# Optimization experiments

Hardware: AMD Instinct MI355X
Metric: run time of the kernel (lower is better)

The kernel has to match this reference:

```python
import jax, jax.numpy as jnp
import numpy as np

N = 100000
E = 1600000
F_IN = 128
H = 128
C = 2


def setup_inputs() -> dict:
    key = jax.random.key(0)
    ks = jax.random.split(key, 12)
    s = lambda fan_in: 1.0 / np.sqrt(fan_in)
    inp = {
        "x": jax.random.normal(ks[0], (N, F_IN), dtype=jnp.float32),
        "edge_index": jax.random.randint(ks[1], (2, E), 0, N, dtype=jnp.int32),
        "edge_weight": jax.random.uniform(ks[2], (E,), dtype=jnp.float32),
        # first_lin: features_num -> hidden
        "W_first": jax.random.uniform(ks[3], (F_IN, H), minval=-s(F_IN), maxval=s(F_IN)),
        "b_first": jnp.zeros((H,), jnp.float32),
        # GRUCell (torch layout: [3*H, H] for ih and hh)
        "W_ih": jax.random.uniform(ks[4], (3 * H, H), minval=-s(H), maxval=s(H)),
        "b_ih": jax.random.uniform(ks[5], (3 * H,), minval=-s(H), maxval=s(H)),
        "W_hh": jax.random.uniform(ks[6], (3 * H, H), minval=-s(H), maxval=s(H)),
        "b_hh": jax.random.uniform(ks[7], (3 * H,), minval=-s(H), maxval=s(H)),
        # lin1: hidden -> hidden
        "W_lin1": jax.random.uniform(ks[8], (H, H), minval=-s(H), maxval=s(H)),
        "b_lin1": jnp.zeros((H,), jnp.float32),
        # out: hidden -> num_class
        "W_out": jax.random.uniform(ks[9], (H, C), minval=-s(H), maxval=s(H)),
        "b_out": jnp.zeros((C,), jnp.float32),
    }
    return inp


def _gated_conv(x, edge_index, edge_weight):
    # gather source node features, scale by edge weight, scatter-add to dst
    src, dst = edge_index[0], edge_index[1]
    msg = x[src] * edge_weight[:, None]           # [E, H]
    return jax.ops.segment_sum(msg, dst, num_segments=N)  # [N, H]


def _gru_cell(inp, hid, W_ih, b_ih, W_hh, b_hh):
    gi = inp @ W_ih.T + b_ih                      # [N, 3H]
    gh = hid @ W_hh.T + b_hh                      # [N, 3H]
    i_r, i_z, i_n = jnp.split(gi, 3, axis=-1)
    h_r, h_z, h_n = jnp.split(gh, 3, axis=-1)
    r = jax.nn.sigmoid(i_r + h_r)
    z = jax.nn.sigmoid(i_z + h_z)
    n = jnp.tanh(i_n + r * h_n)
    return (1.0 - z) * n + z * hid


def reference(x, edge_index, edge_weight, W_first, b_first, W_ih, b_ih,
              W_hh, b_hh, W_lin1, b_lin1, W_out, b_out):
    x = x @ W_first + b_first                     # [N, H] (dropout: eval mode no-op)
    h = x
    x = _gated_conv(x, edge_index, edge_weight)
    x = _gru_cell(x, h, W_ih, b_ih, W_hh, b_hh)
    x = x @ W_lin1 + b_lin1
    x = _gated_conv(x, edge_index, edge_weight)
    x = _gru_cell(x, h, W_ih, b_ih, W_hh, b_hh)
    logits = x @ W_out + b_out                    # [N, C]
    return jax.nn.log_softmax(logits, axis=-1)
```

## Files before the change

### kernel.cpp

```cpp
#include <hip/hip_runtime.h>
#include <hip/hip_bf16.h>

#define H 128
#define SCAN_T 256
#define SCAN_I 8
#define SCAN_CHUNK (SCAN_T * SCAN_I)

typedef __bf16 bf16_t;
typedef __attribute__((ext_vector_type(2))) __bf16 bf16x2;
typedef __attribute__((ext_vector_type(8))) __bf16 bf16x8;
typedef __attribute__((ext_vector_type(4))) float f32x4;

static_assert(sizeof(bf16x8) == 16, "bf16x8 must be 16 bytes");

__device__ inline bf16x8 load_a_frag_f32(const float* __restrict__ A, int row, int koff) {
    const float4* p = (const float4*)(A + (size_t)row * H + koff);
    float4 v0 = p[0], v1 = p[1];
    bf16x8 r;
    r[0] = (bf16_t)v0.x; r[1] = (bf16_t)v0.y; r[2] = (bf16_t)v0.z; r[3] = (bf16_t)v0.w;
    r[4] = (bf16_t)v1.x; r[5] = (bf16_t)v1.y; r[6] = (bf16_t)v1.z; r[7] = (bf16_t)v1.w;
    return r;
}

__global__ void prep_weights(const float* __restrict__ Wf,  const float* __restrict__ Wih,
                             const float* __restrict__ Whh, const float* __restrict__ Wl1,
                             bf16_t* __restrict__ wfT, bf16_t* __restrict__ wih,
                             bf16_t* __restrict__ whh, bf16_t* __restrict__ wl1T) {
    int i = blockIdx.x * blockDim.x + threadIdx.x;
    if (i < 128 * 128) {
        int c = i >> 7, k = i & 127;
        wfT[i]  = (bf16_t)Wf[k * 128 + c];
        wl1T[i] = (bf16_t)Wl1[k * 128 + c];
    }
    if (i < 384 * 128) {
        wih[i] = (bf16_t)Wih[i];
        whh[i] = (bf16_t)Whh[i];
    }
}

__global__ void hist_kernel(const int* __restrict__ ei, int* __restrict__ deg, int nE) {
    int e = blockIdx.x * blockDim.x + threadIdx.x;
    if (e < nE) atomicAdd(&deg[ei[nE + e]], 1);
}

__global__ __launch_bounds__(SCAN_T) void scan1_kernel(
    const int* __restrict__ deg, int* __restrict__ rowptr, int* __restrict__ bsum, int n) {
    __shared__ int s[SCAN_T];
    int base = blockIdx.x * SCAN_CHUNK + threadIdx.x * SCAN_I;
    int v[SCAN_I];
    int sum = 0;
    for (int j = 0; j < SCAN_I; ++j) {
        int idx = base + j;
        v[j] = (idx < n) ? deg[idx] : 0;
        sum += v[j];
    }
    s[threadIdx.x] = sum;
    __syncthreads();
    for (int off = 1; off < SCAN_T; off <<= 1) {
        int t = (threadIdx.x >= off) ? s[threadIdx.x - off] : 0;
        __syncthreads();
        s[threadIdx.x] += t;
        __syncthreads();
    }
    int run = s[threadIdx.x] - sum;
    for (int j = 0; j < SCAN_I; ++j) {
        int idx = base + j;
        if (idx < n) rowptr[idx] = run;
        run += v[j];
    }
    if (threadIdx.x == SCAN_T - 1) bsum[blockIdx.x] = s[SCAN_T - 1];
}

__global__ __launch_bounds__(SCAN_T) void scan2_kernel(int* __restrict__ bsum, int nb) {
    __shared__ int s[SCAN_T];
    int v = (threadIdx.x < nb) ? bsum[threadIdx.x] : 0;
    s[threadIdx.x] = v;
    __syncthreads();
    for (int off = 1; off < SCAN_T; off <<= 1) {
        int t = (threadIdx.x >= off) ? s[threadIdx.x - off] : 0;
        __syncthreads();
        s[threadIdx.x] += t;
        __syncthreads();
    }
    if (threadIdx.x < nb) bsum[threadIdx.x] = s[threadIdx.x] - v;
}

__global__ void scan3_kernel(int* __restrict__ rowptr, int* __restrict__ cursor,
                             const int* __restrict__ bsum, int n, int nE) {
    int idx = blockIdx.x * blockDim.x + threadIdx.x;
    if (idx < n) {
        int val = rowptr[idx] + bsum[idx / SCAN_CHUNK];
        rowptr[idx] = val;
        cursor[idx] = val;
    }
    if (idx == 0) rowptr[n] = nE;
}

__global__ void scatter_kernel(const int* __restrict__ ei, const float* __restrict__ ew,
                               int* __restrict__ cursor, int2* __restrict__ srcw, int nE) {
    int e = blockIdx.x * blockDim.x + threadIdx.x;
    if (e < nE) {
        int src = ei[e], dst = ei[nE + e];
        float w = ew[e];
        int pos = atomicAdd(&cursor[dst], 1);
        srcw[pos] = make_int2(src, __float_as_int(w));
    }
}

__device__ inline void conv_fma(float* acc, uint4 u, float w) {
    acc[0] += __uint_as_float(u.x << 16) * w;
    acc[1] += __uint_as_float(u.x & 0xffff0000u) * w;
    acc[2] += __uint_as_float(u.y << 16) * w;
    acc[3] += __uint_as_float(u.y & 0xffff0000u) * w;
    acc[4] += __uint_as_float(u.z << 16) * w;
    acc[5] += __uint_as_float(u.z & 0xffff0000u) * w;
    acc[6] += __uint_as_float(u.w << 16) * w;
    acc[7] += __uint_as_float(u.w & 0xffff0000u) * w;
}

__global__ __launch_bounds__(256) void conv_csr_kernel(
    const bf16_t* __restrict__ xb, const int* __restrict__ rowptr,
    const int2* __restrict__ srcw, bf16_t* __restrict__ agg, int n) {
    int lane = threadIdx.x & 63;
    int d = (blockIdx.x * blockDim.x + threadIdx.x) >> 6;
    if (d >= n) return;
    int q = lane >> 4;
    int l = lane & 15;
    int beg = rowptr[d], end = rowptr[d + 1];

    float acc[8];
    #pragma unroll
    for (int i = 0; i < 8; ++i) acc[i] = 0.f;

    int e = beg + q;
    for (; e + 4 < end; e += 8) {
        int2 sw0 = srcw[e];
        int2 sw1 = srcw[e + 4];
        uint4 u0 = *(const uint4*)(xb + (size_t)sw0.x * H + l * 8);
        uint4 u1 = *(const uint4*)(xb + (size_t)sw1.x * H + l * 8);
        conv_fma(acc, u0, __int_as_float(sw0.y));
        conv_fma(acc, u1, __int_as_float(sw1.y));
    }
    if (e < end) {
        int2 sw = srcw[e];
        uint4 u = *(const uint4*)(xb + (size_t)sw.x * H + l * 8);
        conv_fma(acc, u, __int_as_float(sw.y));
    }

    #pragma unroll
    for (int i = 0; i < 8; ++i) {
        acc[i] += __shfl_xor(acc[i], 16);
        acc[i] += __shfl_xor(acc[i], 32);
    }
    if (q == 0) {
        bf16x8 r;
        #pragma unroll
        for (int i = 0; i < 8; ++i) r[i] = (bf16_t)acc[i];
        *(bf16x8*)(agg + (size_t)d * H + l * 8) = r;
    }
}

__global__ __launch_bounds__(256) void lin_first_kernel(
    const float* __restrict__ A, const bf16_t* __restrict__ Bt,
    const float* __restrict__ bias, float* __restrict__ outf,
    bf16_t* __restrict__ outb, int n) {
    int wid = threadIdx.x >> 6, lane = threadIdx.x & 63;
    int r0 = (blockIdx.x * 4 + wid) * 32;
    if (r0 >= n) return;
    int lrow = lane & 15, lk8 = (lane >> 4) * 8;

    bf16x8 a[2][4];
    for (int rt = 0; rt < 2; ++rt) {
        int row = r0 + rt * 16 + lrow;
        if (row >= n) row = n - 1;
        for (int t = 0; t < 4; ++t) a[rt][t] = load_a_frag_f32(A, row, t * 32 + lk8);
    }
    for (int ct = 0; ct < 8; ++ct) {
        int c0 = ct * 16;
        f32x4 acc0 = {0.f, 0.f, 0.f, 0.f}, acc1 = {0.f, 0.f, 0.f, 0.f};
        const bf16_t* bp = Bt + (size_t)(c0 + lrow) * H + lk8;
        for (int t = 0; t < 4; ++t) {
            bf16x8 b = *(const bf16x8*)(bp + t * 32);
            acc0 = __builtin_amdgcn_mfma_f32_16x16x32_bf16(a[0][t], b, acc0, 0, 0, 0);
            acc1 = __builtin_amdgcn_mfma_f32_16x16x32_bf16(a[1][t], b, acc1, 0, 0, 0);
        }
        int col = c0 + lrow;
        float bv = bias[col];
        for (int r = 0; r < 4; ++r) {
            int row0 = r0 + (lane >> 4) * 4 + r;
            float v0 = acc0[r] + bv;
            if (row0 < n) { outf[(size_t)row0 * H + col] = v0; outb[(size_t)row0 * H + col] = (bf16_t)v0; }
            int row1 = row0 + 16;
            float v1 = acc1[r] + bv;
            if (row1 < n) { outf[(size_t)row1 * H + col] = v1; outb[(size_t)row1 * H + col] = (bf16_t)v1; }
        }
    }
}

__global__ __launch_bounds__(256) void lin_mid_kernel(
    const bf16_t* __restrict__ A, const bf16_t* __restrict__ Bt,
    const float* __restrict__ bias, bf16_t* __restrict__ out, int n) {
    int wid = threadIdx.x >> 6, lane = threadIdx.x & 63;
    int r0 = (blockIdx.x * 4 + wid) * 32;
    if (r0 >= n) return;
    int lrow = lane & 15, lk8 = (lane >> 4) * 8;

    bf16x8 a[2][4];
    for (int rt = 0; rt < 2; ++rt) {
        int row = r0 + rt * 16 + lrow;
        if (row >= n) row = n - 1;
        for (int t = 0; t < 4; ++t)
            a[rt][t] = *(const bf16x8*)(A + (size_t)row * H + t * 32 + lk8);
    }
    for (int ct = 0; ct < 8; ++ct) {
        int c0 = ct * 16;
        f32x4 acc0 = {0.f, 0.f, 0.f, 0.f}, acc1 = {0.f, 0.f, 0.f, 0.f};
        const bf16_t* bp = Bt + (size_t)(c0 + lrow) * H + lk8;
        for (int t = 0; t < 4; ++t) {
            bf16x8 b = *(const bf16x8*)(bp + t * 32);
            acc0 = __builtin_amdgcn_mfma_f32_16x16x32_bf16(a[0][t], b, acc0, 0, 0, 0);
            acc1 = __builtin_amdgcn_mfma_f32_16x16x32_bf16(a[1][t], b, acc1, 0, 0, 0);
        }
        int col = c0 + lrow;
        float bv = bias[col];
        for (int r = 0; r < 4; ++r) {
            int row0 = r0 + (lane >> 4) * 4 + r;
            if (row0 < n) out[(size_t)row0 * H + col] = (bf16_t)(acc0[r] + bv);
            int row1 = row0 + 16;
            if (row1 < n) out[(size_t)row1 * H + col] = (bf16_t)(acc1[r] + bv);
        }
    }
}

template<bool LOGITS>
__global__ __launch_bounds__(256) void gru_kernel(
    const bf16_t* __restrict__ inp, const bf16_t* __restrict__ hidb,
    const float* __restrict__ hidf,
    const bf16_t* __restrict__ Wih, const bf16_t* __restrict__ Whh,
    const float* __restrict__ bih, const float* __restrict__ bhh,
    bf16_t* __restrict__ out, const float* __restrict__ Wo,
    const float* __restrict__ bo, float* __restrict__ logits, int n) {
    int wid = threadIdx.x >> 6, lane = threadIdx.x & 63;
    int r0 = (blockIdx.x * 4 + wid) * 32;
    if (r0 >= n) return;
    int lrow = lane & 15, lk8 = (lane >> 4) * 8;

    bf16x8 ai[2][4], ah[2][4];
    for (int rt = 0; rt < 2; ++rt) {
        int row = r0 + rt * 16 + lrow;
        if (row >= n) row = n - 1;
        for (int t = 0; t < 4; ++t) {
            ai[rt][t] = *(const bf16x8*)(inp  + (size_t)row * H + t * 32 + lk8);
            ah[rt][t] = *(const bf16x8*)(hidb + (size_t)row * H + t * 32 + lk8);
        }
    }

    float s0[2][4], s1[2][4];
    if (LOGITS) {
        for (int rt = 0; rt < 2; ++rt)
            for (int r = 0; r < 4; ++r) { s0[rt][r] = 0.f; s1[rt][r] = 0.f; }
    }

    for (int ct = 0; ct < 8; ++ct) {
        int c0 = ct * 16;
        int col = c0 + lrow;
        f32x4 air[2], aiz[2], ain[2], ahr[2], ahz[2], ahn[2];
        for (int rt = 0; rt < 2; ++rt) {
            air[rt] = (f32x4){0.f,0.f,0.f,0.f}; aiz[rt] = (f32x4){0.f,0.f,0.f,0.f};
            ain[rt] = (f32x4){0.f,0.f,0.f,0.f}; ahr[rt] = (f32x4){0.f,0.f,0.f,0.f};
            ahz[rt] = (f32x4){0.f,0.f,0.f,0.f}; ahn[rt] = (f32x4){0.f,0.f,0.f,0.f};
        }
        const bf16_t* pir = Wih + (size_t)(col)       * H + lk8;
        const bf16_t* piz = Wih + (size_t)(128 + col) * H + lk8;
        const bf16_t* pin = Wih + (size_t)(256 + col) * H + lk8;
        const bf16_t* phr = Whh + (size_t)(col)       * H + lk8;
        const bf16_t* phz = Whh + (size_t)(128 + col) * H + lk8;
        const bf16_t* phn = Whh + (size_t)(256 + col) * H + lk8;
        for (int t = 0; t < 4; ++t) {
            bf16x8 bir = *(const bf16x8*)(pir + t * 32);
            bf16x8 biz = *(const bf16x8*)(piz + t * 32);
            bf16x8 bin = *(const bf16x8*)(pin + t * 32);
            bf16x8 bhr = *(const bf16x8*)(phr + t * 32);
            bf16x8 bhz = *(const bf16x8*)(phz + t * 32);
            bf16x8 bhn = *(const bf16x8*)(phn + t * 32);
            for (int rt = 0; rt < 2; ++rt) {
                air[rt] = __builtin_amdgcn_mfma_f32_16x16x32_bf16(ai[rt][t], bir, air[rt], 0, 0, 0);
                aiz[rt] = __builtin_amdgcn_mfma_f32_16x16x32_bf16(ai[rt][t], biz, aiz[rt], 0, 0, 0);
                ain[rt] = __builtin_amdgcn_mfma_f32_16x16x32_bf16(ai[rt][t], bin, ain[rt], 0, 0, 0);
                ahr[rt] = __builtin_amdgcn_mfma_f32_16x16x32_bf16(ah[rt][t], bhr, ahr[rt], 0, 0, 0);
                ahz[rt] = __builtin_amdgcn_mfma_f32_16x16x32_bf16(ah[rt][t], bhz, ahz[rt], 0, 0, 0);
                ahn[rt] = __builtin_amdgcn_mfma_f32_16x16x32_bf16(ah[rt][t], bhn, ahn[rt], 0, 0, 0);
            }
        }
        float b_ir = bih[col], b_iz = bih[128 + col], b_in = bih[256 + col];
        float b_hr = bhh[col], b_hz = bhh[128 + col], b_hn = bhh[256 + col];
        float w0 = 0.f, w1 = 0.f;
        if (LOGITS) { float2 wv = *(const float2*)(Wo + col * 2); w0 = wv.x; w1 = wv.y; }
        for (int rt = 0; rt < 2; ++rt) {
            for (int r = 0; r < 4; ++r) {
                int row = r0 + rt * 16 + (lane >> 4) * 4 + r;
                float irv = air[rt][r] + b_ir, hrv = ahr[rt][r] + b_hr;
                float izv = aiz[rt][r] + b_iz, hzv = ahz[rt][r] + b_hz;
                float inv = ain[rt][r] + b_in, hnv = ahn[rt][r] + b_hn;
                float rg = 1.f / (1.f + __expf(-(irv + hrv)));
                float zg = 1.f / (1.f + __expf(-(izv + hzv)));
                float xx = inv + rg * hnv;
                float ng = 2.f / (1.f + __expf(-2.f * xx)) - 1.f;
                bool ok = (row < n);
                float hv = ok ? hidf[(size_t)row * H + col] : 0.f;
                float hout = (1.f - zg) * ng + zg * hv;
                if (LOGITS) {
                    s0[rt][r] += hout * w0;
                    s1[rt][r] += hout * w1;
                } else if (ok) {
                    out[(size_t)row * H + col] = (bf16_t)hout;
                }
            }
        }
    }

    if (LOGITS) {
        for (int m = 1; m < 16; m <<= 1) {
            for (int rt = 0; rt < 2; ++rt)
                for (int r = 0; r < 4; ++r) {
                    s0[rt][r] += __shfl_xor(s0[rt][r], m);
                    s1[rt][r] += __shfl_xor(s1[rt][r], m);
                }
        }
        if ((lane & 15) == 0) {
            float bo0 = bo[0], bo1 = bo[1];
            for (int rt = 0; rt < 2; ++rt)
                for (int r = 0; r < 4; ++r) {
                    int row = r0 + rt * 16 + (lane >> 4) * 4 + r;
                    if (row < n) {
                        float l0 = s0[rt][r] + bo0, l1 = s1[rt][r] + bo1;
                        float mx = fmaxf(l0, l1);
                        float lse = mx + __logf(__expf(l0 - mx) + __expf(l1 - mx));
                        logits[(size_t)row * 2]     = l0 - lse;
                        logits[(size_t)row * 2 + 1] = l1 - lse;
                    }
                }
        }
    }
}

extern "C" void kernel_launch(void* const* d_in, const int* in_sizes, int n_in,
                              void* d_out, int out_size, void* d_ws, size_t ws_size,
                              hipStream_t stream) {
    const float* x   = (const float*)d_in[0];
    const int*   ei  = (const int*)d_in[1];
    const float* ew  = (const float*)d_in[2];
    const float* Wf  = (const float*)d_in[3];
    const float* bf  = (const float*)d_in[4];
    const float* Wih = (const float*)d_in[5];
    const float* bih = (const float*)d_in[6];
    const float* Whh = (const float*)d_in[7];
    const float* bhh = (const float*)d_in[8];
    const float* Wl1 = (const float*)d_in[9];
    const float* bl1 = (const float*)d_in[10];
    const float* Wo  = (const float*)d_in[11];
    const float* bo  = (const float*)d_in[12];

    int n  = in_sizes[0] / H;
    int nE = in_sizes[2];

    float* hbuf   = (float*)d_ws;
    bf16_t* hbufb = (bf16_t*)(hbuf + (size_t)n * H);
    bf16_t* b1b   = hbufb + (size_t)n * H;
    bf16_t* b2b   = b1b + (size_t)n * H;
    bf16_t* wfT   = b2b + (size_t)n * H;
    bf16_t* wih   = wfT + 128 * 128;
    bf16_t* whh   = wih + 384 * 128;
    bf16_t* wl1T  = whh + 384 * 128;
    int* deg    = (int*)(wl1T + 128 * 128);
    int* rowptr = deg + n;
    int* cursor = rowptr + (n + 1);
    int2* srcw  = (int2*)((char*)(cursor + n) + ((size_t)(-(intptr_t)(cursor + n)) & 7));

    int gemmGrid = (n + 127) / 128;
    int nScanBlocks = (n + SCAN_CHUNK - 1) / SCAN_CHUNK;

    prep_weights<<<192, 256, 0, stream>>>(Wf, Wih, Whh, Wl1, wfT, wih, whh, wl1T);
    hipMemsetAsync(deg, 0, (size_t)n * sizeof(int), stream);
    hist_kernel<<<(nE + 255) / 256, 256, 0, stream>>>(ei, deg, nE);
    scan1_kernel<<<nScanBlocks, SCAN_T, 0, stream>>>(deg, rowptr, cursor, n);
    scan2_kernel<<<1, SCAN_T, 0, stream>>>(cursor, nScanBlocks);
    scan3_kernel<<<(n + 255) / 256, 256, 0, stream>>>(rowptr, deg, cursor, n, nE);
    scatter_kernel<<<(nE + 255) / 256, 256, 0, stream>>>(ei, ew, deg, srcw, nE);

    lin_first_kernel<<<gemmGrid, 256, 0, stream>>>(x, wfT, bf, hbuf, hbufb, n);
    conv_csr_kernel<<<(n + 3) / 4, 256, 0, stream>>>(hbufb, rowptr, srcw, b1b, n);
    gru_kernel<false><<<gemmGrid, 256, 0, stream>>>(b1b, hbufb, hbuf, wih, whh, bih, bhh,
                                                    b1b, nullptr, nullptr, nullptr, n);
    lin_mid_kernel<<<gemmGrid, 256, 0, stream>>>(b1b, wl1T, bl1, b2b, n);
    conv_csr_kernel<<<(n + 3) / 4, 256, 0, stream>>>(b2b, rowptr, srcw, b1b, n);
    gru_kernel<true><<<gemmGrid, 256, 0, stream>>>(b1b, hbufb, hbuf, wih, whh, bih, bhh,
                                                   nullptr, Wo, bo, (float*)d_out, n);
}
```

Baseline: 610.6 us.

## Stage weight matrices in swizzled LDS for linear and GRU MFMA kernels

The linear kernels now copy the whole 128x128 bf16 weight matrix into XOR-swizzled shared memory once per block and read MFMA B fragments from LDS instead of global memory. The GRU kernel double-buffers per-column-tile slices of the six gate weight blocks in LDS, prefetching the next slice into registers while the current one is computed. This targets repeated global/L2 weight fetches by every wave. In exchange it adds 32-48KB of LDS per block, which may lower occupancy, plus block-wide barriers. The early return for out-of-range waves is removed so every thread reaches the barriers.

New measurement: 539.1 us. 11.7% less time.

```diff
diff --git a/kernel.cpp b/kernel.cpp
--- a/kernel.cpp
+++ b/kernel.cpp
@@ -160,14 +160,24 @@
     }
 }
 
+
 __global__ __launch_bounds__(256) void lin_first_kernel(
     const float* __restrict__ A, const bf16_t* __restrict__ Bt,
     const float* __restrict__ bias, float* __restrict__ outf,
     bf16_t* __restrict__ outb, int n) {
-    int wid = threadIdx.x >> 6, lane = threadIdx.x & 63;
+    __shared__ __align__(16) unsigned char wlds[32768];
+    int tid = threadIdx.x;
+    int wid = tid >> 6, lane = tid & 63;
     int r0 = (blockIdx.x * 4 + wid) * 32;
-    if (r0 >= n) return;
-    int lrow = lane & 15, lk8 = (lane >> 4) * 8;
+    int lrow = lane & 15, lq = lane >> 4, lk8 = lq * 8;
+
+    #pragma unroll
+    for (int i = 0; i < 8; ++i) {
+        int g = i * 256 + tid;
+        int row = g >> 4, seg = g & 15;
+        uint4 v = *(const uint4*)(Bt + row * 128 + seg * 8);
+        *(uint4*)(&wlds[row * 256 + ((seg * 16) ^ ((row & 7) << 4))]) = v;
+    }
 
     bf16x8 a[2][4];
     for (int rt = 0; rt < 2; ++rt) {
@@ -175,19 +185,23 @@
         if (row >= n) row = n - 1;
         for (int t = 0; t < 4; ++t) a[rt][t] = load_a_frag_f32(A, row, t * 32 + lk8);
     }
+    __syncthreads();
+
     for (int ct = 0; ct < 8; ++ct) {
         int c0 = ct * 16;
         f32x4 acc0 = {0.f, 0.f, 0.f, 0.f}, acc1 = {0.f, 0.f, 0.f, 0.f};
-        const bf16_t* bp = Bt + (size_t)(c0 + lrow) * H + lk8;
+        int rbase = (c0 + lrow) * 256;
+        int sw = (lrow & 7) << 4;
+        #pragma unroll
         for (int t = 0; t < 4; ++t) {
-            bf16x8 b = *(const bf16x8*)(bp + t * 32);
+            bf16x8 b = *(const bf16x8*)(&wlds[rbase + ((t * 64 + lq * 16) ^ sw)]);
             acc0 = __builtin_amdgcn_mfma_f32_16x16x32_bf16(a[0][t], b, acc0, 0, 0, 0);
             acc1 = __builtin_amdgcn_mfma_f32_16x16x32_bf16(a[1][t], b, acc1, 0, 0, 0);
         }
         int col = c0 + lrow;
         float bv = bias[col];
         for (int r = 0; r < 4; ++r) {
-            int row0 = r0 + (lane >> 4) * 4 + r;
+            int row0 = r0 + lq * 4 + r;
             float v0 = acc0[r] + bv;
             if (row0 < n) { outf[(size_t)row0 * H + col] = v0; outb[(size_t)row0 * H + col] = (bf16_t)v0; }
             int row1 = row0 + 16;
@@ -200,10 +214,19 @@
 __global__ __launch_bounds__(256) void lin_mid_kernel(
     const bf16_t* __restrict__ A, const bf16_t* __restrict__ Bt,
     const float* __restrict__ bias, bf16_t* __restrict__ out, int n) {
-    int wid = threadIdx.x >> 6, lane = threadIdx.x & 63;
+    __shared__ __align__(16) unsigned char wlds[32768];
+    int tid = threadIdx.x;
+    int wid = tid >> 6, lane = tid & 63;
     int r0 = (blockIdx.x * 4 + wid) * 32;
-    if (r0 >= n) return;
-    int lrow = lane & 15, lk8 = (lane >> 4) * 8;
+    int lrow = lane & 15, lq = lane >> 4, lk8 = lq * 8;
+
+    #pragma unroll
+    for (int i = 0; i < 8; ++i) {
+        int g = i * 256 + tid;
+        int row = g >> 4, seg = g & 15;
+        uint4 v = *(const uint4*)(Bt + row * 128 + seg * 8);
+        *(uint4*)(&wlds[row * 256 + ((seg * 16) ^ ((row & 7) << 4))]) = v;
+    }
 
     bf16x8 a[2][4];
     for (int rt = 0; rt < 2; ++rt) {
@@ -212,19 +235,23 @@
         for (int t = 0; t < 4; ++t)
             a[rt][t] = *(const bf16x8*)(A + (size_t)row * H + t * 32 + lk8);
     }
+    __syncthreads();
+
     for (int ct = 0; ct < 8; ++ct) {
         int c0 = ct * 16;
         f32x4 acc0 = {0.f, 0.f, 0.f, 0.f}, acc1 = {0.f, 0.f, 0.f, 0.f};
-        const bf16_t* bp = Bt + (size_t)(c0 + lrow) * H + lk8;
+        int rbase = (c0 + lrow) * 256;
+        int sw = (lrow & 7) << 4;
+        #pragma unroll
         for (int t = 0; t < 4; ++t) {
-            bf16x8 b = *(const bf16x8*)(bp + t * 32);
+            bf16x8 b = *(const bf16x8*)(&wlds[rbase + ((t * 64 + lq * 16) ^ sw)]);
             acc0 = __builtin_amdgcn_mfma_f32_16x16x32_bf16(a[0][t], b, acc0, 0, 0, 0);
             acc1 = __builtin_amdgcn_mfma_f32_16x16x32_bf16(a[1][t], b, acc1, 0, 0, 0);
         }
         int col = c0 + lrow;
         float bv = bias[col];
         for (int r = 0; r < 4; ++r) {
-            int row0 = r0 + (lane >> 4) * 4 + r;
+            int row0 = r0 + lq * 4 + r;
             if (row0 < n) out[(size_t)row0 * H + col] = (bf16_t)(acc0[r] + bv);
             int row1 = row0 + 16;
             if (row1 < n) out[(size_t)row1 * H + col] = (bf16_t)(acc1[r] + bv);
@@ -240,10 +267,37 @@
     const float* __restrict__ bih, const float* __restrict__ bhh,
     bf16_t* __restrict__ out, const float* __restrict__ Wo,
     const float* __restrict__ bo, float* __restrict__ logits, int n) {
-    int wid = threadIdx.x >> 6, lane = threadIdx.x & 63;
+    __shared__ __align__(16) unsigned char wlds[2][6 * 4096];
+    int tid = threadIdx.x;
+    int wid = tid >> 6, lane = tid & 63;
     int r0 = (blockIdx.x * 4 + wid) * 32;
-    if (r0 >= n) return;
-    int lrow = lane & 15, lk8 = (lane >> 4) * 8;
+    int lrow = lane & 15, lq = lane >> 4, lk8 = lq * 8;
+
+    int srow = tid >> 4;
+    int sseg = tid & 15;
+    int s_src_off = srow * 128 + sseg * 8;
+    int s_lds_off = srow * 256 + ((sseg * 16) ^ ((srow & 7) << 4));
+
+    uint4 streg[6];
+    auto stage_load = [&](int ct) {
+        const bf16_t* b0 = Wih + (size_t)(ct * 16) * 128;
+        const bf16_t* b1 = Wih + (size_t)(128 + ct * 16) * 128;
+        const bf16_t* b2 = Wih + (size_t)(256 + ct * 16) * 128;
+        const bf16_t* b3 = Whh + (size_t)(ct * 16) * 128;
+        const bf16_t* b4 = Whh + (size_t)(128 + ct * 16) * 128;
+        const bf16_t* b5 = Whh + (size_t)(256 + ct * 16) * 128;
+        streg[0] = *(const uint4*)(b0 + s_src_off);
+        streg[1] = *(const uint4*)(b1 + s_src_off);
+        streg[2] = *(const uint4*)(b2 + s_src_off);
+        streg[3] = *(const uint4*)(b3 + s_src_off);
+        streg[4] = *(const uint4*)(b4 + s_src_off);
+        streg[5] = *(const uint4*)(b5 + s_src_off);
+    };
+    auto stage_write = [&](int buf) {
+        #pragma unroll
+        for (int s = 0; s < 6; ++s)
+            *(uint4*)(&wlds[buf][s * 4096 + s_lds_off]) = streg[s];
+    };
 
     bf16x8 ai[2][4], ah[2][4];
     for (int rt = 0; rt < 2; ++rt) {
@@ -255,6 +309,10 @@
         }
     }
 
+    stage_load(0);
+    stage_write(0);
+    __syncthreads();
+
     float s0[2][4], s1[2][4];
     if (LOGITS) {
         for (int rt = 0; rt < 2; ++rt)
@@ -262,27 +320,27 @@
     }
 
     for (int ct = 0; ct < 8; ++ct) {
-        int c0 = ct * 16;
-        int col = c0 + lrow;
+        if (ct + 1 < 8) stage_load(ct + 1);
+        const unsigned char* wb = wlds[ct & 1];
+        int col = ct * 16 + lrow;
+
         f32x4 air[2], aiz[2], ain[2], ahr[2], ahz[2], ahn[2];
         for (int rt = 0; rt < 2; ++rt) {
             air[rt] = (f32x4){0.f,0.f,0.f,0.f}; aiz[rt] = (f32x4){0.f,0.f,0.f,0.f};
             ain[rt] = (f32x4){0.f,0.f,0.f,0.f}; ahr[rt] = (f32x4){0.f,0.f,0.f,0.f};
             ahz[rt] = (f32x4){0.f,0.f,0.f,0.f}; ahn[rt] = (f32x4){0.f,0.f,0.f,0.f};
         }
-        const bf16_t* pir = Wih + (size_t)(col)       * H + lk8;
-        const bf16_t* piz = Wih + (size_t)(128 + col) * H + lk8;
-        const bf16_t* pin = Wih + (size_t)(256 + col) * H + lk8;
-        const bf16_t* phr = Whh + (size_t)(col)       * H + lk8;
-        const bf16_t* phz = Whh + (size_t)(128 + col) * H + lk8;
-        const bf16_t* phn = Whh + (size_t)(256 + col) * H + lk8;
+        int rbase = lrow * 256;
+        int sw = (lrow & 7) << 4;
+        #pragma unroll
         for (int t = 0; t < 4; ++t) {
-            bf16x8 bir = *(const bf16x8*)(pir + t * 32);
-            bf16x8 biz = *(const bf16x8*)(piz + t * 32);
-            bf16x8 bin = *(const bf16x8*)(pin + t * 32);
-            bf16x8 bhr = *(const bf16x8*)(phr + t * 32);
-            bf16x8 bhz = *(const bf16x8*)(phz + t * 32);
-            bf16x8 bhn = *(const bf16x8*)(phn + t * 32);
+            int roff = rbase + ((t * 64 + lq * 16) ^ sw);
+            bf16x8 bir = *(const bf16x8*)(wb + 0 * 4096 + roff);
+            bf16x8 biz = *(const bf16x8*)(wb + 1 * 4096 + roff);
+            bf16x8 bin = *(const bf16x8*)(wb + 2 * 4096 + roff);
+            bf16x8 bhr = *(const bf16x8*)(wb + 3 * 4096 + roff);
+            bf16x8 bhz = *(const bf16x8*)(wb + 4 * 4096 + roff);
+            bf16x8 bhn = *(const bf16x8*)(wb + 5 * 4096 + roff);
             for (int rt = 0; rt < 2; ++rt) {
                 air[rt] = __builtin_amdgcn_mfma_f32_16x16x32_bf16(ai[rt][t], bir, air[rt], 0, 0, 0);
                 aiz[rt] = __builtin_amdgcn_mfma_f32_16x16x32_bf16(ai[rt][t], biz, aiz[rt], 0, 0, 0);
@@ -292,13 +350,14 @@
                 ahn[rt] = __builtin_amdgcn_mfma_f32_16x16x32_bf16(ah[rt][t], bhn, ahn[rt], 0, 0, 0);
             }
         }
+
         float b_ir = bih[col], b_iz = bih[128 + col], b_in = bih[256 + col];
         float b_hr = bhh[col], b_hz = bhh[128 + col], b_hn = bhh[256 + col];
         float w0 = 0.f, w1 = 0.f;
         if (LOGITS) { float2 wv = *(const float2*)(Wo + col * 2); w0 = wv.x; w1 = wv.y; }
         for (int rt = 0; rt < 2; ++rt) {
             for (int r = 0; r < 4; ++r) {
-                int row = r0 + rt * 16 + (lane >> 4) * 4 + r;
+                int row = r0 + rt * 16 + lq * 4 + r;
                 float irv = air[rt][r] + b_ir, hrv = ahr[rt][r] + b_hr;
                 float izv = aiz[rt][r] + b_iz, hzv = ahz[rt][r] + b_hz;
                 float inv = ain[rt][r] + b_in, hnv = ahn[rt][r] + b_hn;
@@ -317,6 +376,11 @@
                 }
             }
         }
+
+        if (ct + 1 < 8) {
+            stage_write((ct + 1) & 1);
+            __syncthreads();
+        }
     }
 
     if (LOGITS) {
@@ -327,11 +391,11 @@
                     s1[rt][r] += __shfl_xor(s1[rt][r], m);
                 }
         }
-        if ((lane & 15) == 0) {
+        if (lrow == 0) {
             float bo0 = bo[0], bo1 = bo[1];
             for (int rt = 0; rt < 2; ++rt)
                 for (int r = 0; r < 4; ++r) {
-                    int row = r0 + rt * 16 + (lane >> 4) * 4 + r;
+                    int row = r0 + rt * 16 + lq * 4 + r;
                     if (row < n) {
                         float l0 = s0[rt][r] + bo0, l1 = s1[rt][r] + bo1;
                         float mx = fmaxf(l0, l1);
```
